# Kernel optimization log

Measured on AMD Instinct MI355X. Metric: run time of the kernel, lower is better.

The kernel has to match this reference:

```python
import jax, jax.numpy as jnp
import numpy as np


def setup_inputs() -> dict:
    key = jax.random.key(0)
    k1, k2, k3 = jax.random.split(key, 3)
    B, R, Din, D = 4096, 4096, 1024, 1024
    x = jax.random.normal(k1, (B, Din), dtype=jnp.float32)
    refs = jax.random.normal(k2, (R, Din), dtype=jnp.float32)
    W = jax.random.normal(k3, (Din, D), dtype=jnp.float32) * (1.0 / np.sqrt(Din))
    b = jnp.zeros((D,), dtype=jnp.float32)
    return {"x": x, "refs": refs, "W": W, "b": b}


def reference(x, refs, W, b) -> jnp.ndarray:
    # feature extractor (linear stand-in for the CResNet embedding)
    vin = x @ W + b          # (B, D)
    vrefs = refs @ W + b     # (R, D)
    # compute_degradation_metric: mean_r ||vin_b - vref_r||^2
    # = ||vin||^2 + mean_r ||vref_r||^2 - 2 * vin @ mean_r(vref_r)
    # Same math as the naive broadcast-sub-square-sum-mean, GEMM-friendly form.
    sq_in = jnp.sum(vin * vin, axis=1)                 # (B,)
    mean_sq_ref = jnp.mean(jnp.sum(vrefs * vrefs, axis=1))  # scalar
    mean_ref = jnp.mean(vrefs, axis=0)                 # (D,)
    cross = vin @ mean_ref                             # (B,)
    degradation_metric = sq_in + mean_sq_ref - 2.0 * cross
    return degradation_metric
```

## Files before the change

### kernel.cpp

```cpp
#include <hip/hip_runtime.h>
#include <hip/hip_bf16.h>
#include <stdint.h>


typedef __attribute__((ext_vector_type(8))) short short8;
typedef __attribute__((ext_vector_type(4))) float f32x4;

__device__ __forceinline__ short f2bf(float f) {
  uint32_t u = __builtin_bit_cast(uint32_t, f);
  uint32_t r = (u + 0x7fffu + ((u >> 16) & 1u)) >> 16;
  return (short)r;
}
__device__ __forceinline__ float bf2f(short s) {
  uint32_t u = ((uint32_t)(uint16_t)s) << 16;
  return __builtin_bit_cast(float, u);
}

#define WS_WT 16777216u
#define WS_CP 18874368u
#define WS_CS 20971520u
#define WS_XP 20979712u
#define WS_RR 20996096u

__global__ __launch_bounds__(256) void k_prep(
    const float* __restrict__ refs, const float* __restrict__ W,
    short* __restrict__ wt, float* __restrict__ cspart, float* __restrict__ zacc) {
  __shared__ short tile[64][68];
  const int b = blockIdx.x, t = threadIdx.x;
  if (b < 512) {
    const int rblk = b;
    const int c0 = t * 4;
    float s0 = 0.f, s1 = 0.f, s2 = 0.f, s3 = 0.f;
    for (int r = rblk * 8; r < rblk * 8 + 8; ++r) {
      float4 v = *(const float4*)&refs[(size_t)r * 1024 + c0];
      s0 += v.x; s1 += v.y; s2 += v.z; s3 += v.w;
    }
    cspart[rblk * 1024 + c0 + 0] = s0;
    cspart[rblk * 1024 + c0 + 1] = s1;
    cspart[rblk * 1024 + c0 + 2] = s2;
    cspart[rblk * 1024 + c0 + 3] = s3;
  } else if (b < 768) {
    const int tb = b - 512;
    const int tk = (tb >> 4) * 64, tn = (tb & 15) * 64;
    const int kk = t >> 4, nn4 = (t & 15) * 4;
#pragma unroll
    for (int p = 0; p < 4; ++p) {
      int k = kk + p * 16;
      float4 v = *(const float4*)&W[(size_t)(tk + k) * 1024 + tn + nn4];
      tile[nn4 + 0][k] = f2bf(v.x);
      tile[nn4 + 1][k] = f2bf(v.y);
      tile[nn4 + 2][k] = f2bf(v.z);
      tile[nn4 + 3][k] = f2bf(v.w);
    }
    __syncthreads();
    const int nn = t >> 4, kk4 = (t & 15) * 4;
#pragma unroll
    for (int p = 0; p < 4; ++p) {
      int n = nn + p * 16;
      uint32_t lo = (uint16_t)tile[n][kk4 + 0] | ((uint32_t)(uint16_t)tile[n][kk4 + 1] << 16);
      uint32_t hi = (uint16_t)tile[n][kk4 + 2] | ((uint32_t)(uint16_t)tile[n][kk4 + 3] << 16);
      *(uint2*)&wt[(size_t)(tn + n) * 1024 + tk + kk4] = make_uint2(lo, hi);
    }
  } else {
    const int i = (b - 768) * 256 + t;
    ((float4*)zacc)[i]        = make_float4(0.f, 0.f, 0.f, 0.f);
    ((float4*)zacc)[i + 1024] = make_float4(0.f, 0.f, 0.f, 0.f);
  }
}

__global__ void k_colsum(const float* __restrict__ cspart, float* __restrict__ colsum) {
  __shared__ float sh[8][32];
  const int t = threadIdx.x;
  const int c = t & 31, pg = t >> 5;
  const int k = blockIdx.x * 32 + c;
  float s = 0.f;
  for (int i = 0; i < 64; ++i) s += cspart[(size_t)(pg * 64 + i) * 1024 + k];
  sh[pg][c] = s;
  __syncthreads();
  if (t < 32) {
    float tot = 0.f;
#pragma unroll
    for (int g = 0; g < 8; ++g) tot += sh[g][t];
    colsum[blockIdx.x * 32 + t] = tot;
  }
}

__global__ __launch_bounds__(512, 4) void k_main(
    const float* __restrict__ X, const float* __restrict__ R,
    const short* __restrict__ Wt, const float* __restrict__ bias,
    const float* __restrict__ colsum, float* __restrict__ xpart,
    float* __restrict__ refrow) {
  __shared__ __align__(16) short As[2][128 * 64];
  __shared__ __align__(16) short Bs[2][128 * 64];
  __shared__ __align__(16) short cs_lds[1024];
  const int t = threadIdx.x;
  const int w = t >> 6, l = t & 63;
  const int wr = w >> 2, wc = w & 3;
  const int bx = blockIdx.x;
  const int nt = bx >> 6;
  const int mt = bx & 63;
  const bool is_x = (mt < 32);
  const float* Am = is_x ? X : R;
  const int m0 = (is_x ? mt : (mt - 32)) * 128;
  const int n0 = nt * 128;

  const int srow = t >> 3;
  const int sslot = t & 7;
  const int arow = t >> 4;
  const int acol = (t & 15) * 4;
  const int asl = (t & 15) >> 1, ah = t & 1;

  f32x4 acc[4][2] = {};
  f32x4 acc_t[2] = {};
  float4 areg[4];

  auto stageB = [&](int buf, int kt) {
    const int k0 = kt * 64;
#pragma unroll
    for (int issue = 0; issue < 2; ++issue) {
      const int row = srow + issue * 64;
      const int sg = sslot ^ (row & 7);
      const short* gb = Wt + ((size_t)(n0 + row) * 1024 + k0 + sg * 8);
      char* lb = (char*)&Bs[buf][0] + issue * 8192 + w * 1024;
      __builtin_amdgcn_global_load_lds(
          (const __attribute__((address_space(1))) unsigned int*)gb,
          (__attribute__((address_space(3))) unsigned int*)lb, 16, 0, 0);
    }
  };
  auto loadA = [&](int kt) {
    const int k0 = kt * 64;
#pragma unroll
    for (int i = 0; i < 4; ++i) {
      const int r = arow + i * 32;
      areg[i] = *(const float4*)&Am[(size_t)(m0 + r) * 1024 + k0 + acol];
    }
  };
  auto writeA = [&](int buf) {
#pragma unroll
    for (int i = 0; i < 4; ++i) {
      const int r = arow + i * 32;
      uint32_t lo, hi;
      asm("v_cvt_pk_bf16_f32 %0, %1, %2" : "=v"(lo) : "v"(areg[i].x), "v"(areg[i].y));
      asm("v_cvt_pk_bf16_f32 %0, %1, %2" : "=v"(hi) : "v"(areg[i].z), "v"(areg[i].w));
      char* p = (char*)&As[buf][0] + r * 128 + (((asl ^ (r & 7)) * 16) + ah * 8);
      *(uint2*)p = make_uint2(lo, hi);
    }
  };

  stageB(0, 0);
  stageB(1, 1);
  loadA(0);
  writeA(0);
  loadA(1);
  if (t < 128) {
    float4 c0 = *(const float4*)&colsum[t * 8];
    float4 c1 = *(const float4*)&colsum[t * 8 + 4];
    uint32_t p0, p1, p2, p3;
    asm("v_cvt_pk_bf16_f32 %0, %1, %2" : "=v"(p0) : "v"(c0.x), "v"(c0.y));
    asm("v_cvt_pk_bf16_f32 %0, %1, %2" : "=v"(p1) : "v"(c0.z), "v"(c0.w));
    asm("v_cvt_pk_bf16_f32 %0, %1, %2" : "=v"(p2) : "v"(c1.x), "v"(c1.y));
    asm("v_cvt_pk_bf16_f32 %0, %1, %2" : "=v"(p3) : "v"(c1.z), "v"(c1.w));
    *(uint4*)&cs_lds[t * 8] = make_uint4(p0, p1, p2, p3);
  }

  for (int kt = 0; kt < 16; ++kt) {
    asm volatile("s_waitcnt lgkmcnt(0)" ::: "memory");
    __builtin_amdgcn_s_barrier();
    const int cur = kt & 1;
#pragma unroll
    for (int kk = 0; kk < 2; ++kk) {
      short8 af[4], bfr[2], csf;
      csf = *(const short8*)&cs_lds[kt * 64 + kk * 32 + (l >> 4) * 8];
#pragma unroll
      for (int i = 0; i < 4; ++i) {
        const int ra = wr * 64 + i * 16 + (l & 15);
        const int s = (l >> 4) + kk * 4;
        af[i] = *(const short8*)&As[cur][ra * 64 + ((s ^ (ra & 7)) * 8)];
      }
#pragma unroll
      for (int j = 0; j < 2; ++j) {
        const int rbw = wc * 32 + j * 16 + (l & 15);
        const int s = (l >> 4) + kk * 4;
        bfr[j] = *(const short8*)&Bs[cur][rbw * 64 + ((s ^ (rbw & 7)) * 8)];
      }
      __builtin_amdgcn_s_setprio(1);
#pragma unroll
      for (int i = 0; i < 4; ++i)
#pragma unroll
        for (int j = 0; j < 2; ++j)
          acc[i][j] = __builtin_amdgcn_mfma_f32_16x16x32_bf16(af[i], bfr[j], acc[i][j], 0, 0, 0);
#pragma unroll
      for (int j = 0; j < 2; ++j)
        acc_t[j] = __builtin_amdgcn_mfma_f32_16x16x32_bf16(csf, bfr[j], acc_t[j], 0, 0, 0);
      __builtin_amdgcn_s_setprio(0);
    }
    __builtin_amdgcn_s_barrier();
    if (kt + 2 < 16) stageB(cur, kt + 2);
    if (kt + 1 < 16) writeA((kt + 1) & 1);
    if (kt + 2 < 16) loadA(kt + 2);
  }

  float bv[2], tvv[2];
#pragma unroll
  for (int n2 = 0; n2 < 2; ++n2) {
    const int col = n0 + wc * 32 + n2 * 16 + (l & 15);
    bv[n2] = bias[col];
    tvv[n2] = acc_t[n2][0] * (1.0f / 4096.0f) + bv[n2];
  }
#pragma unroll
  for (int m4 = 0; m4 < 4; ++m4) {
#pragma unroll
    for (int j = 0; j < 4; ++j) {
      float sq = 0.f, cr = 0.f;
#pragma unroll
      for (int n2 = 0; n2 < 2; ++n2) {
        const float v = acc[m4][n2][j] + bv[n2];
        sq += v * v;
        cr += v * tvv[n2];
      }
#pragma unroll
      for (int off = 1; off < 16; off <<= 1) {
        sq += __shfl_xor(sq, off, 64);
        cr += __shfl_xor(cr, off, 64);
      }
      if ((l & 15) == 0) {
        const int rm = m0 + wr * 64 + m4 * 16 + (l >> 4) * 4 + j;
        if (is_x) atomicAdd(&xpart[rm], sq - 2.0f * cr);
        else      atomicAdd(&refrow[rm], sq);
      }
    }
  }
}

__global__ void k_tail(const float* __restrict__ refrow, const float* __restrict__ xpart,
                       float* __restrict__ out) {
  __shared__ float sh[16];
  const int t = threadIdx.x;
  float s = 0.f;
  for (int i = t; i < 4096; i += 1024) s += refrow[i];
#pragma unroll
  for (int off = 32; off; off >>= 1) s += __shfl_down(s, off, 64);
  const int w = t >> 6, l = t & 63;
  if (l == 0) sh[w] = s;
  __syncthreads();
  if (t == 0) {
    float tot = 0.f;
#pragma unroll
    for (int i = 0; i < 16; ++i) tot += sh[i];
    sh[0] = tot * (1.0f / 4096.0f);
  }
  __syncthreads();
  const float ms = sh[0];
  for (int i = t; i < 4096; i += 1024) out[i] = xpart[i] + ms;
}

extern "C" void kernel_launch(void* const* d_in, const int* in_sizes, int n_in,
                              void* d_out, int out_size, void* d_ws, size_t ws_size,
                              hipStream_t stream) {
  const float* x    = (const float*)d_in[0];
  const float* refs = (const float*)d_in[1];
  const float* W    = (const float*)d_in[2];
  const float* bias = (const float*)d_in[3];
  float* out = (float*)d_out;
  char* ws = (char*)d_ws;

  short* wt     = (short*)(ws + WS_WT);
  float* cspart = (float*)(ws + WS_CP);
  float* colsum = (float*)(ws + WS_CS);
  float* xpart  = (float*)(ws + WS_XP);
  float* refrow = (float*)(ws + WS_RR);

  hipLaunchKernelGGL(k_prep, dim3(772), dim3(256), 0, stream, refs, W, wt, cspart, xpart);
  hipLaunchKernelGGL(k_colsum, dim3(32), dim3(256), 0, stream, cspart, colsum);
  hipLaunchKernelGGL(k_main, dim3(512), dim3(512), 0, stream, x, refs, wt, bias, colsum, xpart, refrow);
  hipLaunchKernelGGL(k_tail, dim3(1), dim3(1024), 0, stream, refrow, xpart, out);
}
```

Before: 46.13 us.

## Overlap A-tile conversion with MFMA and skip redundant colsum MFMAs

Moves the A-tile register-to-LDS write and next global load to the start of each k-iteration, and uses a partial vmcnt wait so global loads stay in flight while MFMAs run. The colsum (mean-ref) MFMAs now run only for x blocks and only in the wr==0 warps, with results shared to other warps through LDS after the loop. The epilogue combines the sq and cross terms before the shuffle reduction, halving shuffles, and ref blocks skip the cross computation. This adds a __syncthreads and depends on the vmcnt count being correct for the load ordering.

```diff
diff --git a/kernel.cpp b/kernel.cpp
--- a/kernel.cpp
+++ b/kernel.cpp
@@ -147,12 +147,12 @@
     }
   };
 
+  loadA(0);
   stageB(0, 0);
   stageB(1, 1);
-  loadA(0);
   writeA(0);
   loadA(1);
-  if (t < 128) {
+  if (is_x && t < 128) {
     float4 c0 = *(const float4*)&colsum[t * 8];
     float4 c1 = *(const float4*)&colsum[t * 8 + 4];
     uint32_t p0, p1, p2, p3;
@@ -164,13 +164,15 @@
   }
 
   for (int kt = 0; kt < 16; ++kt) {
-    asm volatile("s_waitcnt lgkmcnt(0)" ::: "memory");
+    if (kt < 15) asm volatile("s_waitcnt vmcnt(6) lgkmcnt(0)" ::: "memory");
+    else         asm volatile("s_waitcnt vmcnt(0) lgkmcnt(0)" ::: "memory");
     __builtin_amdgcn_s_barrier();
     const int cur = kt & 1;
+    if (kt + 1 < 16) writeA((kt + 1) & 1);
+    if (kt + 2 < 16) loadA(kt + 2);
 #pragma unroll
     for (int kk = 0; kk < 2; ++kk) {
-      short8 af[4], bfr[2], csf;
-      csf = *(const short8*)&cs_lds[kt * 64 + kk * 32 + (l >> 4) * 8];
+      short8 af[4], bfr[2];
 #pragma unroll
       for (int i = 0; i < 4; ++i) {
         const int ra = wr * 64 + i * 16 + (l & 15);
@@ -189,44 +191,66 @@
 #pragma unroll
         for (int j = 0; j < 2; ++j)
           acc[i][j] = __builtin_amdgcn_mfma_f32_16x16x32_bf16(af[i], bfr[j], acc[i][j], 0, 0, 0);
-#pragma unroll
-      for (int j = 0; j < 2; ++j)
-        acc_t[j] = __builtin_amdgcn_mfma_f32_16x16x32_bf16(csf, bfr[j], acc_t[j], 0, 0, 0);
+      if (is_x && wr == 0) {
+        short8 csf = *(const short8*)&cs_lds[kt * 64 + kk * 32 + (l >> 4) * 8];
+#pragma unroll
+        for (int j = 0; j < 2; ++j)
+          acc_t[j] = __builtin_amdgcn_mfma_f32_16x16x32_bf16(csf, bfr[j], acc_t[j], 0, 0, 0);
+      }
       __builtin_amdgcn_s_setprio(0);
     }
     __builtin_amdgcn_s_barrier();
     if (kt + 2 < 16) stageB(cur, kt + 2);
-    if (kt + 1 < 16) writeA((kt + 1) & 1);
-    if (kt + 2 < 16) loadA(kt + 2);
+  }
+
+  float* tpan = (float*)cs_lds;
+  if (is_x) {
+    if (wr == 0 && l < 16) {
+      tpan[wc * 32 + l]      = acc_t[0][0];
+      tpan[wc * 32 + 16 + l] = acc_t[1][0];
+    }
+    __syncthreads();
   }
 
   float bv[2], tvv[2];
 #pragma unroll
   for (int n2 = 0; n2 < 2; ++n2) {
-    const int col = n0 + wc * 32 + n2 * 16 + (l & 15);
-    bv[n2] = bias[col];
-    tvv[n2] = acc_t[n2][0] * (1.0f / 4096.0f) + bv[n2];
+    const int ci = wc * 32 + n2 * 16 + (l & 15);
+    bv[n2] = bias[n0 + ci];
+    tvv[n2] = is_x ? (tpan[ci] * (1.0f / 4096.0f) + bv[n2]) : 0.f;
   }
 #pragma unroll
   for (int m4 = 0; m4 < 4; ++m4) {
 #pragma unroll
     for (int j = 0; j < 4; ++j) {
-      float sq = 0.f, cr = 0.f;
-#pragma unroll
-      for (int n2 = 0; n2 < 2; ++n2) {
-        const float v = acc[m4][n2][j] + bv[n2];
-        sq += v * v;
-        cr += v * tvv[n2];
-      }
-#pragma unroll
-      for (int off = 1; off < 16; off <<= 1) {
-        sq += __shfl_xor(sq, off, 64);
-        cr += __shfl_xor(cr, off, 64);
-      }
-      if ((l & 15) == 0) {
-        const int rm = m0 + wr * 64 + m4 * 16 + (l >> 4) * 4 + j;
-        if (is_x) atomicAdd(&xpart[rm], sq - 2.0f * cr);
-        else      atomicAdd(&refrow[rm], sq);
+      if (is_x) {
+        float sq = 0.f, cr = 0.f;
+#pragma unroll
+        for (int n2 = 0; n2 < 2; ++n2) {
+          const float v = acc[m4][n2][j] + bv[n2];
+          sq += v * v;
+          cr += v * tvv[n2];
+        }
+        float comb = sq - 2.0f * cr;
+#pragma unroll
+        for (int off = 1; off < 16; off <<= 1) comb += __shfl_xor(comb, off, 64);
+        if ((l & 15) == 0) {
+          const int rm = m0 + wr * 64 + m4 * 16 + (l >> 4) * 4 + j;
+          atomicAdd(&xpart[rm], comb);
+        }
+      } else {
+        float sq = 0.f;
+#pragma unroll
+        for (int n2 = 0; n2 < 2; ++n2) {
+          const float v = acc[m4][n2][j] + bv[n2];
+          sq += v * v;
+        }
+#pragma unroll
+        for (int off = 1; off < 16; off <<= 1) sq += __shfl_xor(sq, off, 64);
+        if ((l & 15) == 0) {
+          const int rm = m0 + wr * 64 + m4 * 16 + (l >> 4) * 4 + j;
+          atomicAdd(&refrow[rm], sq);
+        }
       }
     }
   }
```

Result: faster. 44.57 us (median of 2 runs) (-3.4%).
